# Kernel optimization log

Measured on AMD Instinct MI355X. Metric: run time of the kernel, lower is better.

## Reference

```python
import jax, jax.numpy as jnp
import numpy as np

B, C, H, W = 4, 256, 128, 256
NUM_CODES = 256  # codebook rows; dim_code == C


def setup_inputs() -> dict:
    key = jax.random.key(0)
    k_feat, k_code = jax.random.split(key)
    feature = jax.random.normal(k_feat, (B, C, H, W), dtype=jnp.float32)
    codebook = jax.random.normal(k_code, (NUM_CODES, C), dtype=jnp.float32)
    return {"feature": feature, "codebook": codebook}


def reference(feature, codebook):
    # Faithful to ComminPub.sender core:
    #   weights = (feature_expand * codebooks).sum(dim=2) / (codebooks*codebooks).sum(dim=2)
    # expressed as a contraction over C instead of materializing [B,N,C,H,W].
    code_norm = jnp.sum(codebook * codebook, axis=1)          # [N]
    weights = jnp.einsum('bchw,nc->bnhw', feature, codebook)   # [B,N,H,W]
    weights = weights / code_norm[None, :, None, None]
    # fc_after_rbdc reconstruction: einsum('b n h w, n c -> b c h w', weights, codebook)
    recon = jnp.einsum('bnhw,nc->bchw', weights, codebook)     # [B,C,H,W]
    return recon
```

## Files before the change

### kernel.cpp

```cpp
#include <hip/hip_runtime.h>
#include <hip/hip_bf16.h>
#include <cstdint>

#define CDIM   256
#define NCODES 256
#define HWB    32768
#define BATCH  4
#define BM     128
#define BN     64
#define BK     32
#define NKC    8

typedef __bf16 bf16x8 __attribute__((ext_vector_type(8)));
typedef float  f32x4  __attribute__((ext_vector_type(4)));

#define GLDS(g, l)                                                         \
    __builtin_amdgcn_global_load_lds(                                      \
        (const __attribute__((address_space(1))) void*)(g),                \
        (__attribute__((address_space(3))) void*)(l), 16, 0, 0)

__global__ __launch_bounds__(256) void prep_kernel(
    const float* __restrict__ cb, __bf16* __restrict__ Mb) {
    __shared__ float g[NCODES];
    const int i    = blockIdx.x;
    const int tid  = threadIdx.x;
    const int lane = tid & 63;
    const int w    = tid >> 6;

#pragma unroll 4
    for (int r = 0; r < 64; ++r) {
        const int n = w * 64 + r;
        const float* row = cb + n * CDIM;
        float v0 = row[lane], v1 = row[lane + 64],
              v2 = row[lane + 128], v3 = row[lane + 192];
        float s = v0 * v0 + v1 * v1 + v2 * v2 + v3 * v3;
#pragma unroll
        for (int off = 32; off > 0; off >>= 1) s += __shfl_down(s, off, 64);
        if (lane == 0) g[n] = cb[n * CDIM + i] / s;
    }
    __syncthreads();

    float acc = 0.f;
#pragma unroll 8
    for (int n = 0; n < NCODES; ++n)
        acc += g[n] * cb[n * CDIM + tid];
    Mb[i * CDIM + tid] = (__bf16)acc;
}

__global__ __launch_bounds__(64, 2) void recon_kernel(
    const float* __restrict__ feat, const __bf16* __restrict__ Mb,
    float* __restrict__ out) {
    __shared__ __align__(16) __bf16 Albuf[2][BM * BK];
    __shared__ __align__(16) float  Blbuf[2][BK * BN];

    const int lane = threadIdx.x;
    const int quad = lane >> 4;
    const int l16  = lane & 15;

    const int p0 = blockIdx.x * BN;
    const int c0 = blockIdx.y * BM;
    const int b  = blockIdx.z;

    const float* fbase = feat + ((size_t)b * CDIM) * HWB + p0;
    float*       obase = out  + ((size_t)b * CDIM) * HWB + p0;

    const __bf16* asrc = Mb + (c0 + (lane >> 2)) * CDIM + (lane & 3) * 8;
    const float*  bsrc = fbase + (size_t)(lane >> 4) * HWB + (lane & 15) * 4;

    auto issue = [&](int s) {
        const int buf = s & 1;
#pragma unroll
        for (int h = 0; h < 8; ++h)
            GLDS(asrc + (h * 16) * CDIM + s * BK, &Albuf[buf][h * 512]);
#pragma unroll
        for (int g = 0; g < 8; ++g)
            GLDS(bsrc + (size_t)(s * BK + g * 4) * HWB, &Blbuf[buf][g * 256]);
    };

    f32x4 acc[8][4];
#pragma unroll
    for (int mt = 0; mt < 8; ++mt)
#pragma unroll
        for (int nt = 0; nt < 4; ++nt)
            acc[mt][nt] = (f32x4){0.f, 0.f, 0.f, 0.f};

    issue(0);
    issue(1);

#pragma unroll
    for (int s = 0; s < NKC; ++s) {
        const int buf = s & 1;
        if (s < NKC - 1) asm volatile("s_waitcnt vmcnt(16)" ::: "memory");
        else             asm volatile("s_waitcnt vmcnt(0)"  ::: "memory");

        bf16x8 af[8];
#pragma unroll
        for (int mt = 0; mt < 8; ++mt)
            af[mt] = *(const bf16x8*)&Albuf[buf][(mt * 16 + l16) * BK + quad * 8];

        bf16x8 bfr[4];
#pragma unroll
        for (int nt = 0; nt < 4; ++nt) {
            bf16x8 t;
#pragma unroll
            for (int j = 0; j < 8; ++j)
                t[j] = (__bf16)Blbuf[buf][(quad * 8 + j) * BN + nt * 16 + l16];
            bfr[nt] = t;
        }

        asm volatile("s_waitcnt lgkmcnt(0)" ::: "memory");
        if (s + 2 < NKC) issue(s + 2);

#pragma unroll
        for (int mt = 0; mt < 8; ++mt)
#pragma unroll
            for (int nt = 0; nt < 4; ++nt)
                acc[mt][nt] = __builtin_amdgcn_mfma_f32_16x16x32_bf16(
                    af[mt], bfr[nt], acc[mt][nt], 0, 0, 0);
    }

#pragma unroll
    for (int mt = 0; mt < 8; ++mt) {
#pragma unroll
        for (int r = 0; r < 4; ++r) {
            const int c = c0 + mt * 16 + quad * 4 + r;
            float* orow = obase + (size_t)c * HWB + l16;
#pragma unroll
            for (int nt = 0; nt < 4; ++nt)
                orow[nt * 16] = acc[mt][nt][r];
        }
    }
}

extern "C" void kernel_launch(void* const* d_in, const int* in_sizes, int n_in,
                              void* d_out, int out_size, void* d_ws, size_t ws_size,
                              hipStream_t stream) {
    const float* feat = (const float*)d_in[0];
    const float* cb   = (const float*)d_in[1];
    float* out = (float*)d_out;

    __bf16* Mb = (__bf16*)d_ws;

    prep_kernel<<<NCODES, 256, 0, stream>>>(cb, Mb);

    dim3 grid(HWB / BN, CDIM / BM, BATCH);
    recon_kernel<<<grid, 64, 0, stream>>>(feat, Mb, out);
}
```

Baseline: 295.2 us.

## Use 4-wave blocks covering all channels to share feature tiles across waves

Recon kernel now launches 256-thread blocks where each of four waves computes 64 output channels, so a block covers all 256 channels and each feature tile is loaded once instead of once per channel half. Feature loads switch to 4-byte global-to-LDS transfers into a padded row stride (65) to reduce LDS bank conflicts on the transposing reads. Barriers are added for cross-wave buffer sharing. The trade-off is more, narrower load instructions and barrier synchronisation costs.

```diff
diff --git a/kernel.cpp b/kernel.cpp
--- a/kernel.cpp
+++ b/kernel.cpp
@@ -6,18 +6,22 @@
 #define NCODES 256
 #define HWB    32768
 #define BATCH  4
-#define BM     128
 #define BN     64
 #define BK     32
 #define NKC    8
+#define BPAD   65
 
 typedef __bf16 bf16x8 __attribute__((ext_vector_type(8)));
 typedef float  f32x4  __attribute__((ext_vector_type(4)));
 
-#define GLDS(g, l)                                                         \
+#define GLDS16(g, l)                                                       \
     __builtin_amdgcn_global_load_lds(                                      \
         (const __attribute__((address_space(1))) void*)(g),                \
         (__attribute__((address_space(3))) void*)(l), 16, 0, 0)
+#define GLDS4(g, l)                                                        \
+    __builtin_amdgcn_global_load_lds(                                      \
+        (const __attribute__((address_space(1))) void*)(g),                \
+        (__attribute__((address_space(3))) void*)(l), 4, 0, 0)
 
 __global__ __launch_bounds__(256) void prep_kernel(
     const float* __restrict__ cb, __bf16* __restrict__ Mb) {
@@ -47,39 +51,46 @@
     Mb[i * CDIM + tid] = (__bf16)acc;
 }
 
-__global__ __launch_bounds__(64, 2) void recon_kernel(
+__global__ __launch_bounds__(256, 3) void recon_kernel(
     const float* __restrict__ feat, const __bf16* __restrict__ Mb,
     float* __restrict__ out) {
-    __shared__ __align__(16) __bf16 Albuf[2][BM * BK];
-    __shared__ __align__(16) float  Blbuf[2][BK * BN];
+    __shared__ __align__(16) __bf16 Albuf[2][CDIM * BK];
+    __shared__ __align__(16) float  Blbuf[2][BK * BPAD];
 
-    const int lane = threadIdx.x;
+    const int tid  = threadIdx.x;
+    const int lane = tid & 63;
+    const int w    = tid >> 6;
     const int quad = lane >> 4;
     const int l16  = lane & 15;
 
     const int p0 = blockIdx.x * BN;
-    const int c0 = blockIdx.y * BM;
-    const int b  = blockIdx.z;
+    const int b  = blockIdx.y;
 
     const float* fbase = feat + ((size_t)b * CDIM) * HWB + p0;
     float*       obase = out  + ((size_t)b * CDIM) * HWB + p0;
 
-    const __bf16* asrc = Mb + (c0 + (lane >> 2)) * CDIM + (lane & 3) * 8;
-    const float*  bsrc = fbase + (size_t)(lane >> 4) * HWB + (lane & 15) * 4;
+    const int a_c  = (lane >> 2);
+    const int a_kq = (lane & 3) * 8;
 
     auto issue = [&](int s) {
         const int buf = s & 1;
 #pragma unroll
-        for (int h = 0; h < 8; ++h)
-            GLDS(asrc + (h * 16) * CDIM + s * BK, &Albuf[buf][h * 512]);
+        for (int i = 0; i < 4; ++i) {
+            const int h = w * 4 + i;
+            const __bf16* src = Mb + (h * 16 + a_c) * CDIM + s * BK + a_kq;
+            GLDS16(src, &Albuf[buf][h * 512]);
+        }
 #pragma unroll
-        for (int g = 0; g < 8; ++g)
-            GLDS(bsrc + (size_t)(s * BK + g * 4) * HWB, &Blbuf[buf][g * 256]);
+        for (int i = 0; i < 8; ++i) {
+            const int r = w * 8 + i;
+            const float* src = fbase + (size_t)(s * BK + r) * HWB + lane;
+            GLDS4(src, &Blbuf[buf][r * BPAD]);
+        }
     };
 
-    f32x4 acc[8][4];
+    f32x4 acc[4][4];
 #pragma unroll
-    for (int mt = 0; mt < 8; ++mt)
+    for (int mt = 0; mt < 4; ++mt)
 #pragma unroll
         for (int nt = 0; nt < 4; ++nt)
             acc[mt][nt] = (f32x4){0.f, 0.f, 0.f, 0.f};
@@ -90,13 +101,15 @@
 #pragma unroll
     for (int s = 0; s < NKC; ++s) {
         const int buf = s & 1;
-        if (s < NKC - 1) asm volatile("s_waitcnt vmcnt(16)" ::: "memory");
+        if (s < NKC - 1) asm volatile("s_waitcnt vmcnt(12)" ::: "memory");
         else             asm volatile("s_waitcnt vmcnt(0)"  ::: "memory");
+        asm volatile("s_barrier" ::: "memory");
 
-        bf16x8 af[8];
+        bf16x8 af[4];
 #pragma unroll
-        for (int mt = 0; mt < 8; ++mt)
-            af[mt] = *(const bf16x8*)&Albuf[buf][(mt * 16 + l16) * BK + quad * 8];
+        for (int mt = 0; mt < 4; ++mt)
+            af[mt] = *(const bf16x8*)
+                &Albuf[buf][(w * 64 + mt * 16 + l16) * BK + quad * 8];
 
         bf16x8 bfr[4];
 #pragma unroll
@@ -104,15 +117,16 @@
             bf16x8 t;
 #pragma unroll
             for (int j = 0; j < 8; ++j)
-                t[j] = (__bf16)Blbuf[buf][(quad * 8 + j) * BN + nt * 16 + l16];
+                t[j] = (__bf16)Blbuf[buf][(quad * 8 + j) * BPAD + nt * 16 + l16];
             bfr[nt] = t;
         }
 
         asm volatile("s_waitcnt lgkmcnt(0)" ::: "memory");
+        asm volatile("s_barrier" ::: "memory");
         if (s + 2 < NKC) issue(s + 2);
 
 #pragma unroll
-        for (int mt = 0; mt < 8; ++mt)
+        for (int mt = 0; mt < 4; ++mt)
 #pragma unroll
             for (int nt = 0; nt < 4; ++nt)
                 acc[mt][nt] = __builtin_amdgcn_mfma_f32_16x16x32_bf16(
@@ -120,10 +134,10 @@
     }
 
 #pragma unroll
-    for (int mt = 0; mt < 8; ++mt) {
+    for (int mt = 0; mt < 4; ++mt) {
 #pragma unroll
         for (int r = 0; r < 4; ++r) {
-            const int c = c0 + mt * 16 + quad * 4 + r;
+            const int c = w * 64 + mt * 16 + quad * 4 + r;
             float* orow = obase + (size_t)c * HWB + l16;
 #pragma unroll
             for (int nt = 0; nt < 4; ++nt)
@@ -143,6 +157,6 @@
 
     prep_kernel<<<NCODES, 256, 0, stream>>>(cb, Mb);
 
-    dim3 grid(HWB / BN, CDIM / BM, BATCH);
-    recon_kernel<<<grid, 64, 0, stream>>>(feat, Mb, out);
+    dim3 grid(HWB / BN, BATCH);
+    recon_kernel<<<grid, 256, 0, stream>>>(feat, Mb, out);
 }
```

After: 292.4 us. Within noise of the previous version (-0.9%).
